# Optimization experiments

Hardware: AMD Instinct MI355X
Metric: run time of the kernel (lower is better)

## Reference

```python
import jax, jax.numpy as jnp
import numpy as np

D_MODEL = 256
N_HEADS = 8
HEAD_DIM = D_MODEL // N_HEADS


def setup_inputs() -> dict:
    key = jax.random.key(0)
    ks = jax.random.split(key, 10)
    B, L, D = 2, 2048, D_MODEL
    s = 1.0 / np.sqrt(D)
    inp = {
        "x": jax.random.normal(ks[0], (B, L, D), dtype=jnp.float32),
        "Wq": jax.random.normal(ks[1], (D, D), dtype=jnp.float32) * s,
        "bq": jnp.zeros((D,), jnp.float32),
        "Wk": jax.random.normal(ks[2], (D, D), dtype=jnp.float32) * s,
        "bk": jnp.zeros((D,), jnp.float32),
        "Wv": jax.random.normal(ks[3], (D, D), dtype=jnp.float32) * s,
        "bv": jnp.zeros((D,), jnp.float32),
        "u": jax.random.normal(ks[4], (N_HEADS, 1, 1), dtype=jnp.float32) * 0.1,
        "Wo": jax.random.normal(ks[5], (D, D), dtype=jnp.float32) * s,
        "bo": jnp.zeros((D,), jnp.float32),
    }
    return inp


def reference(x, Wq, bq, Wk, bk, Wv, bv, u, Wo, bo):
    B, L, D = x.shape
    H, hd = N_HEADS, HEAD_DIM

    def proj(W, b):  # torch Linear: x @ W.T + b -> [B,H,L,hd]
        return (x @ W.T + b).reshape(B, L, H, hd).transpose(0, 2, 1, 3)

    Q, K, V = proj(Wq, bq), proj(Wk, bk), proj(Wv, bv)

    scores = jnp.einsum("bhqd,bhkd->bhqk", Q, K) / np.sqrt(hd)
    attn_series = jax.nn.softmax(scores, axis=-1)  # [B,H,L,L]

    pos = jnp.arange(L, dtype=jnp.float32)
    dist = jnp.abs(pos[None, :] - pos[:, None])  # [L,L]
    # prior per head: exp(-d^2 / (2*(u^2+1e-6))), normalized over last dim
    prior = jnp.exp(-(dist[None] ** 2) / (2.0 * (u ** 2 + 1e-6)))  # [H,L,L]
    prior = prior / (prior.sum(axis=-1, keepdims=True) + 1e-6)

    discrepancy = jnp.abs(attn_series - prior[None]).mean(axis=(1, 2))  # [B,L]

    out = jnp.einsum("bhqk,bhkd->bhqd", attn_series, V)
    out = out.transpose(0, 2, 1, 3).reshape(B, L, D)
    out = out @ Wo.T + bo
    return out, discrepancy
```

## Files before the change

kernel.cpp:

```cpp
#include <hip/hip_runtime.h>
#include <hip/hip_bf16.h>
#include <math.h>

#define LSEQ 2048
#define DMODEL 256
#define NH 8
#define HD 32

typedef __attribute__((ext_vector_type(8))) short bf16x8;
typedef __attribute__((ext_vector_type(4))) float f32x4;

#define MFMA __builtin_amdgcn_mfma_f32_16x16x32_bf16

__device__ __forceinline__ short f2bf(float x) {
  __hip_bfloat16 h = __float2bfloat16(x);
  return __builtin_bit_cast(short, h);
}
__device__ __forceinline__ float bf2f(short s) {
  __hip_bfloat16 h = __builtin_bit_cast(__hip_bfloat16, s);
  return __bfloat162float(h);
}
__device__ __forceinline__ short bftrunc(float x) {
  return (short)(__builtin_bit_cast(unsigned int, x) >> 16);
}
__device__ __forceinline__ float fexp2(float x) {
#if __has_builtin(__builtin_amdgcn_exp2f)
  return __builtin_amdgcn_exp2f(x);
#else
  return __expf(x * 0.6931471805599453f);
#endif
}
__device__ __forceinline__ float flog2(float x) {
#if __has_builtin(__builtin_amdgcn_logf)
  return __builtin_amdgcn_logf(x);
#else
  return __logf(x) * 1.4426950408889634f;
#endif
}

__global__ __launch_bounds__(256) void aux_kernel(
    const float* __restrict__ Wq, const float* __restrict__ Wk,
    const float* __restrict__ Wv, const float* __restrict__ Wo,
    const float* __restrict__ u,
    short* __restrict__ Wch, short* __restrict__ Wcl,
    short* __restrict__ Woh, short* __restrict__ Wol,
    float* __restrict__ Eb, float* __restrict__ Zb,
    float* __restrict__ disc)
{
  __shared__ float Cs[LSEQ];
  __shared__ float part[256];
  const int tid = threadIdx.x;
  if (blockIdx.x < 256) {
    const int i4 = (blockIdx.x * 256 + tid) * 4;
    const float* src; short* dh; short* dl;
    if (i4 < 196608) {
      int row = i4 >> 8, col = i4 & 255;
      const float* W = (row < 256) ? Wq : (row < 512) ? Wk : Wv;
      src = W + (row & 255) * 256 + col; dh = Wch + i4; dl = Wcl + i4;
    } else {
      int j = i4 - 196608; src = Wo + j; dh = Woh + j; dl = Wol + j;
    }
    float4 v = *(const float4*)src;
    short h0 = f2bf(v.x), h1 = f2bf(v.y), h2 = f2bf(v.z), h3 = f2bf(v.w);
    *(short4*)dh = make_short4(h0, h1, h2, h3);
    *(short4*)dl = make_short4(bftrunc(v.x - bf2f(h0)), bftrunc(v.y - bf2f(h1)),
                               bftrunc(v.z - bf2f(h2)), bftrunc(v.w - bf2f(h3)));
    return;
  }
  const int h = blockIdx.x - 256;
  const float uu = u[h];
  const float den = 2.0f * (uu * uu + 1e-6f);
  float e[8]; float run = 0.f;
  const int base = tid * 8;
#pragma unroll
  for (int j = 0; j < 8; ++j) {
    float d = (float)(base + j);
    e[j] = __expf(-(d * d) / den);
    run += e[j];
  }
  part[tid] = run;
  __syncthreads();
  for (int off = 1; off < 256; off <<= 1) {
    float v = (tid >= off) ? part[tid - off] : 0.f;
    __syncthreads();
    part[tid] += v;
    __syncthreads();
  }
  float c = part[tid] - run;
#pragma unroll
  for (int j = 0; j < 8; ++j) {
    c += e[j];
    Cs[base + j] = c;
    Eb[h * LSEQ + base + j] = e[j];
  }
  __syncthreads();
  const float E0 = Cs[0];
  for (int i = tid; i < LSEQ; i += 256) {
    float s = Cs[i] + Cs[LSEQ - 1 - i] - E0;
    Zb[h * LSEQ + i] = 1.0f / (s + 1e-6f);
  }
  for (int i = tid; i < 512; i += 256) disc[h * 512 + i] = 0.f;
}

__global__ __launch_bounds__(256) void qkv_gemm(
    const float* __restrict__ x,
    const short* __restrict__ Bh, const short* __restrict__ Bl,
    const float* __restrict__ bq, const float* __restrict__ bk,
    const float* __restrict__ bv,
    short* __restrict__ Qf, short* __restrict__ Kf, short* __restrict__ Vf)
{
  const int tid = threadIdx.x, w = tid >> 6, lane = tid & 63;
  const int l15 = lane & 15, q4 = lane >> 4;
  const int m0 = blockIdx.x * 64, n0 = blockIdx.y * 64;
  const int mrow = m0 + w * 16 + l15;
  f32x4 acc[4] = {{0,0,0,0},{0,0,0,0},{0,0,0,0},{0,0,0,0}};
  for (int k0 = 0; k0 < 256; k0 += 32) {
    const float* xp = &x[(size_t)mrow * 256 + k0 + q4 * 8];
    float4 a = *(const float4*)xp;
    float4 c = *(const float4*)(xp + 4);
    float av[8] = {a.x,a.y,a.z,a.w,c.x,c.y,c.z,c.w};
    bf16x8 ah, al;
#pragma unroll
    for (int j = 0; j < 8; ++j) {
      short hi = f2bf(av[j]);
      ah[j] = hi;
      al[j] = bftrunc(av[j] - bf2f(hi));
    }
#pragma unroll
    for (int nt = 0; nt < 4; ++nt) {
      const size_t bi = (size_t)(n0 + nt * 16 + l15) * 256 + k0 + q4 * 8;
      bf16x8 bh = *(const bf16x8*)&Bh[bi];
      bf16x8 bl = *(const bf16x8*)&Bl[bi];
      acc[nt] = MFMA(ah, bh, acc[nt], 0, 0, 0);
      acc[nt] = MFMA(al, bh, acc[nt], 0, 0, 0);
      acc[nt] = MFMA(ah, bl, acc[nt], 0, 0, 0);
    }
  }
  const int type = n0 >> 8;
  const int n0l = n0 & 255;
  const float* bias = (type == 0) ? bq : (type == 1) ? bk : bv;
  const float qls = 0.25503489f;
#pragma unroll
  for (int nt = 0; nt < 4; ++nt) {
    const int col = n0l + nt * 16 + l15;
    const float bvv = bias[col];
    const int hh = col >> 5, dloc = col & 31;
#pragma unroll
    for (int r = 0; r < 4; ++r) {
      const int m = m0 + w * 16 + q4 * 4 + r;
      float v = acc[nt][r] + bvv;
      const int bb = m >> 11, mm = m & 2047, rr = mm & 15;
      if (type == 2) {
        const int kt128 = mm >> 7, low7 = mm & 127;
        const int wv = (low7 >> 4) & 3, ph = low7 >> 6;
        const int c = ph * 16 + rr;
        const size_t idx =
          ((((((size_t)bb * 8 + hh) * 16 + kt128) * 4 + wv) * 2 + (dloc >> 4)) * 64
           + (c >> 3) * 16 + (dloc & 15)) * 8 + (c & 7);
        Vf[idx] = f2bf(v);
      } else if (type == 0) {
        const int qblk = mm >> 5, rg = (mm >> 4) & 1;
        const size_t idx =
          (((((size_t)bb * 8 + hh) * 64 + qblk) * 2 + rg) * 64
           + (dloc >> 3) * 16 + rr) * 8 + (dloc & 7);
        Qf[idx] = f2bf(v * qls);
      } else {
        const int g = mm >> 4;
        const size_t idx =
          ((((size_t)bb * 8 + hh) * 128 + g) * 64
           + (dloc >> 3) * 16 + rr) * 8 + (dloc & 7);
        Kf[idx] = f2bf(v);
      }
    }
  }
}

__global__ __launch_bounds__(256) void out_gemm(
    const short* __restrict__ Ah, const short* __restrict__ Al,
    const short* __restrict__ Bh, const short* __restrict__ Bl,
    const float* __restrict__ bias, float* __restrict__ C)
{
  const int tid = threadIdx.x, w = tid >> 6, lane = tid & 63;
  const int l15 = lane & 15, q4 = lane >> 4;
  const int m0 = blockIdx.x * 64, n0 = blockIdx.y * 64;
  const int mrow = m0 + w * 16 + l15;
  f32x4 acc[4] = {{0,0,0,0},{0,0,0,0},{0,0,0,0},{0,0,0,0}};
  for (int k0 = 0; k0 < 256; k0 += 32) {
    bf16x8 ah = *(const bf16x8*)&Ah[(size_t)mrow * 256 + k0 + q4 * 8];
    bf16x8 al = *(const bf16x8*)&Al[(size_t)mrow * 256 + k0 + q4 * 8];
#pragma unroll
    for (int nt = 0; nt < 4; ++nt) {
      const size_t bi = (size_t)(n0 + nt * 16 + l15) * 256 + k0 + q4 * 8;
      bf16x8 bh = *(const bf16x8*)&Bh[bi];
      bf16x8 bl = *(const bf16x8*)&Bl[bi];
      acc[nt] = MFMA(ah, bh, acc[nt], 0, 0, 0);
      acc[nt] = MFMA(al, bh, acc[nt], 0, 0, 0);
      acc[nt] = MFMA(ah, bl, acc[nt], 0, 0, 0);
    }
  }
#pragma unroll
  for (int nt = 0; nt < 4; ++nt) {
    const int col = n0 + nt * 16 + l15;
    const float bvv = bias[col];
#pragma unroll
    for (int r = 0; r < 4; ++r) {
      const int m = m0 + w * 16 + q4 * 4 + r;
      C[(size_t)m * 256 + col] = acc[nt][r] + bvv;
    }
  }
}

__global__ __launch_bounds__(256) void attn_kernel(
    const short* __restrict__ Qf, const short* __restrict__ Kf,
    const short* __restrict__ Vf,
    const float* __restrict__ Eb, const float* __restrict__ Zb,
    short* __restrict__ Ohb, short* __restrict__ Olb,
    float* __restrict__ disc)
{
  __shared__ short Pt[4][32][40];
  __shared__ float Elds[192];
  __shared__ float dcol[LSEQ];
  __shared__ float lpart[4][32];

  const int tid = threadIdx.x, w = tid >> 6, lane = tid & 63;
  const int l15 = lane & 15, q4 = lane >> 4;
  const int flat = blockIdx.x + 64 * (blockIdx.y + 8 * blockIdx.z);
  const int slot = flat >> 3;
  const int g = (flat & 7) | ((slot >> 6) << 3);
  const int h = g & 7, b = g >> 3;
  const int q0 = (slot & 63) * 32;
  const int bh = b * NH + h;

  for (int i = tid; i < LSEQ; i += 256) dcol[i] = 0.f;
  if (tid < 192) Elds[tid] = Eb[h * LSEQ + tid];

  const bf16x8* Qf8 = (const bf16x8*)Qf;
  const bf16x8* Kf8 = (const bf16x8*)Kf;
  const bf16x8* Vf8 = (const bf16x8*)Vf;

  bf16x8 qh[2];
  float iz[2][4];
#pragma unroll
  for (int rg = 0; rg < 2; ++rg) {
    qh[rg] = Qf8[((((size_t)bh * 64 + (q0 >> 5)) * 2 + rg)) * 64 + lane];
#pragma unroll
    for (int r = 0; r < 4; ++r) iz[rg][r] = Zb[h * LSEQ + q0 + rg * 16 + q4 * 4 + r];
  }
  __syncthreads();

  const size_t kfb = (size_t)bh * 128;
  const size_t vfb = (size_t)bh * 16;

  float lac[2][4] = {{0,0,0,0},{0,0,0,0}};
#pragma unroll 2
  for (int kt = 0; kt < LSEQ; kt += 128) {
    bf16x8 k0 = Kf8[(kfb + (kt >> 4) + w) * 64 + lane];
    bf16x8 k1 = Kf8[(kfb + (kt >> 4) + 4 + w) * 64 + lane];
#pragma unroll
    for (int rg = 0; rg < 2; ++rg) {
      f32x4 s0 = {0.f, 0.f, 0.f, 0.f};
      s0 = MFMA(qh[rg], k0, s0, 0, 0, 0);
      f32x4 s1 = {0.f, 0.f, 0.f, 0.f};
      s1 = MFMA(qh[rg], k1, s1, 0, 0, 0);
#pragma unroll
      for (int r = 0; r < 4; ++r) lac[rg][r] += fexp2(s0[r]) + fexp2(s1[r]);
    }
  }
#pragma unroll
  for (int rg = 0; rg < 2; ++rg)
#pragma unroll
    for (int r = 0; r < 4; ++r) {
      float v = lac[rg][r];
      v += __shfl_xor(v, 1); v += __shfl_xor(v, 2);
      v += __shfl_xor(v, 4); v += __shfl_xor(v, 8);
      lac[rg][r] = v;
    }
  if (l15 == 0) {
#pragma unroll
    for (int rg = 0; rg < 2; ++rg)
#pragma unroll
      for (int r = 0; r < 4; ++r) lpart[w][rg * 16 + q4 * 4 + r] = lac[rg][r];
  }
  __syncthreads();
  f32x4 sinit[2];
#pragma unroll
  for (int rg = 0; rg < 2; ++rg)
#pragma unroll
    for (int r = 0; r < 4; ++r) {
      const int qi = rg * 16 + q4 * 4 + r;
      sinit[rg][r] = -flog2(lpart[0][qi] + lpart[1][qi] + lpart[2][qi] + lpart[3][qi]);
    }

  f32x4 oacc[2][2] = {{{0,0,0,0},{0,0,0,0}},{{0,0,0,0},{0,0,0,0}}};
#pragma unroll 2
  for (int kt = 0; kt < LSEQ; kt += 128) {
    bf16x8 kh0 = Kf8[(kfb + (kt >> 4) + w) * 64 + lane];
    bf16x8 kh1 = Kf8[(kfb + (kt >> 4) + 4 + w) * 64 + lane];
    bf16x8 vb[2];
#pragma unroll
    for (int dt = 0; dt < 2; ++dt)
      vb[dt] = Vf8[(((vfb + (kt >> 7)) * 4 + w) * 2 + dt) * 64 + lane];
#pragma unroll
    for (int ph = 0; ph < 2; ++ph) {
      bf16x8 kbh = ph ? kh1 : kh0;
      const int c0 = kt + ph * 64 + w * 16;
      const int kg = c0 + l15;
      const int dd = c0 - q0;
      const bool near = (dd >= -96) && (dd <= 96);
      float dsum = 0.f;
#pragma unroll
      for (int rg = 0; rg < 2; ++rg) {
        f32x4 s = sinit[rg];
        s = MFMA(qh[rg], kbh, s, 0, 0, 0);
#pragma unroll
        for (int r = 0; r < 4; ++r) {
          float p = fexp2(s[r]);
          Pt[w][rg * 16 + q4 * 4 + r][ph * 16 + l15] = bftrunc(p);
          if (near) {
            int qrow = q0 + rg * 16 + q4 * 4 + r;
            int dist = (qrow >= kg) ? (qrow - kg) : (kg - qrow);
            dsum += fabsf(p - Elds[dist] * iz[rg][r]);
          } else {
            dsum += p;
          }
        }
      }
      dsum += __shfl_xor(dsum, 16);
      dsum += __shfl_xor(dsum, 32);
      if (q4 == 0) atomicAdd(&dcol[kg], dsum);
    }
#pragma unroll
    for (int rg = 0; rg < 2; ++rg) {
      bf16x8 pa = *(const bf16x8*)&Pt[w][rg * 16 + l15][q4 * 8];
#pragma unroll
      for (int dt = 0; dt < 2; ++dt)
        oacc[rg][dt] = MFMA(pa, vb[dt], oacc[rg][dt], 0, 0, 0);
    }
  }

  __syncthreads();
  float* Ored = (float*)&Pt[0][0][0];
#pragma unroll
  for (int dt = 0; dt < 2; ++dt) {
#pragma unroll
    for (int rg = 0; rg < 2; ++rg)
#pragma unroll
      for (int r = 0; r < 4; ++r)
        Ored[(w * 32 + rg * 16 + q4 * 4 + r) * 17 + l15] = oacc[rg][dt][r];
    __syncthreads();
    for (int t = tid; t < 512; t += 256) {
      const int q = t >> 4, d = t & 15;
      float v = Ored[(q) * 17 + d] + Ored[(32 + q) * 17 + d] +
                Ored[(64 + q) * 17 + d] + Ored[(96 + q) * 17 + d];
      const size_t oo = ((size_t)b * LSEQ + q0 + q) * DMODEL + h * HD + dt * 16 + d;
      short hi = f2bf(v);
      Ohb[oo] = hi;
      Olb[oo] = bftrunc(v - bf2f(hi));
    }
    __syncthreads();
  }
  const float sc = 1.0f / (float)(NH * LSEQ);
  for (int i = tid; i < LSEQ; i += 256)
    atomicAdd(&disc[(size_t)b * LSEQ + i], dcol[i] * sc);
}

extern "C" void kernel_launch(void* const* d_in, const int* in_sizes, int n_in,
                              void* d_out, int out_size, void* d_ws, size_t ws_size,
                              hipStream_t stream)
{
  const float* x  = (const float*)d_in[0];
  const float* Wq = (const float*)d_in[1];
  const float* bq = (const float*)d_in[2];
  const float* Wk = (const float*)d_in[3];
  const float* bk = (const float*)d_in[4];
  const float* Wv = (const float*)d_in[5];
  const float* bv = (const float*)d_in[6];
  const float* u  = (const float*)d_in[7];
  const float* Wo = (const float*)d_in[8];
  const float* bo = (const float*)d_in[9];

  float* out  = (float*)d_out;
  float* disc = out + (size_t)2 * LSEQ * DMODEL;

  char* w8 = (char*)d_ws;
  const size_t MB = 1u << 20;
  short* Qfb = (short*)(w8);
  short* Kfb = (short*)(w8 + 2 * MB);
  short* Vfb = (short*)(w8 + 4 * MB);
  short* Ohb = (short*)(w8 + 6 * MB);
  short* Olb = (short*)(w8 + 8 * MB);
  short* Wch = (short*)(w8 + 10 * MB);
  short* Wcl = (short*)(w8 + 10 * MB + 393216);
  short* Woh = (short*)(w8 + 10 * MB + 786432);
  short* Wol = (short*)(w8 + 10 * MB + 917504);
  float* Eb  = (float*)(w8 + 11 * MB);
  float* Zb  = (float*)(w8 + 11 * MB + 65536);

  aux_kernel<<<264, 256, 0, stream>>>(Wq, Wk, Wv, Wo, u, Wch, Wcl, Woh, Wol,
                                      Eb, Zb, disc);
  qkv_gemm<<<dim3(64, 12), 256, 0, stream>>>(x, Wch, Wcl, bq, bk, bv,
                                             Qfb, Kfb, Vfb);
  attn_kernel<<<dim3(LSEQ / 32, NH, 2), 256, 0, stream>>>(Qfb, Kfb, Vfb,
                                                          Eb, Zb, Ohb, Olb, disc);
  out_gemm<<<dim3(64, 4), 256, 0, stream>>>(Ohb, Olb, Woh, Wol, bo, out);
}
```

Before: 171.1 us.

## Use single bf16 pass for QKV projection and tighten attention register use

```diff
diff --git a/kernel.cpp b/kernel.cpp
--- a/kernel.cpp
+++ b/kernel.cpp
@@ -42,7 +42,7 @@
     const float* __restrict__ Wq, const float* __restrict__ Wk,
     const float* __restrict__ Wv, const float* __restrict__ Wo,
     const float* __restrict__ u,
-    short* __restrict__ Wch, short* __restrict__ Wcl,
+    short* __restrict__ Wh,
     short* __restrict__ Woh, short* __restrict__ Wol,
     float* __restrict__ Eb, float* __restrict__ Zb,
     float* __restrict__ disc)
@@ -52,19 +52,19 @@
   const int tid = threadIdx.x;
   if (blockIdx.x < 256) {
     const int i4 = (blockIdx.x * 256 + tid) * 4;
-    const float* src; short* dh; short* dl;
     if (i4 < 196608) {
       int row = i4 >> 8, col = i4 & 255;
       const float* W = (row < 256) ? Wq : (row < 512) ? Wk : Wv;
-      src = W + (row & 255) * 256 + col; dh = Wch + i4; dl = Wcl + i4;
+      float4 v = *(const float4*)(W + (row & 255) * 256 + col);
+      *(short4*)(Wh + i4) = make_short4(f2bf(v.x), f2bf(v.y), f2bf(v.z), f2bf(v.w));
     } else {
-      int j = i4 - 196608; src = Wo + j; dh = Woh + j; dl = Wol + j;
-    }
-    float4 v = *(const float4*)src;
-    short h0 = f2bf(v.x), h1 = f2bf(v.y), h2 = f2bf(v.z), h3 = f2bf(v.w);
-    *(short4*)dh = make_short4(h0, h1, h2, h3);
-    *(short4*)dl = make_short4(bftrunc(v.x - bf2f(h0)), bftrunc(v.y - bf2f(h1)),
-                               bftrunc(v.z - bf2f(h2)), bftrunc(v.w - bf2f(h3)));
+      int j = i4 - 196608;
+      float4 v = *(const float4*)(Wo + j);
+      short h0 = f2bf(v.x), h1 = f2bf(v.y), h2 = f2bf(v.z), h3 = f2bf(v.w);
+      *(short4*)(Woh + j) = make_short4(h0, h1, h2, h3);
+      *(short4*)(Wol + j) = make_short4(bftrunc(v.x - bf2f(h0)), bftrunc(v.y - bf2f(h1)),
+                                        bftrunc(v.z - bf2f(h2)), bftrunc(v.w - bf2f(h3)));
+    }
     return;
   }
   const int h = blockIdx.x - 256;
@@ -104,7 +104,7 @@
 
 __global__ __launch_bounds__(256) void qkv_gemm(
     const float* __restrict__ x,
-    const short* __restrict__ Bh, const short* __restrict__ Bl,
+    const short* __restrict__ Bh,
     const float* __restrict__ bq, const float* __restrict__ bk,
     const float* __restrict__ bv,
     short* __restrict__ Qf, short* __restrict__ Kf, short* __restrict__ Vf)
@@ -118,22 +118,14 @@
     const float* xp = &x[(size_t)mrow * 256 + k0 + q4 * 8];
     float4 a = *(const float4*)xp;
     float4 c = *(const float4*)(xp + 4);
-    float av[8] = {a.x,a.y,a.z,a.w,c.x,c.y,c.z,c.w};
-    bf16x8 ah, al;
-#pragma unroll
-    for (int j = 0; j < 8; ++j) {
-      short hi = f2bf(av[j]);
-      ah[j] = hi;
-      al[j] = bftrunc(av[j] - bf2f(hi));
-    }
+    bf16x8 ah;
+    ah[0] = f2bf(a.x); ah[1] = f2bf(a.y); ah[2] = f2bf(a.z); ah[3] = f2bf(a.w);
+    ah[4] = f2bf(c.x); ah[5] = f2bf(c.y); ah[6] = f2bf(c.z); ah[7] = f2bf(c.w);
 #pragma unroll
     for (int nt = 0; nt < 4; ++nt) {
       const size_t bi = (size_t)(n0 + nt * 16 + l15) * 256 + k0 + q4 * 8;
       bf16x8 bh = *(const bf16x8*)&Bh[bi];
-      bf16x8 bl = *(const bf16x8*)&Bl[bi];
       acc[nt] = MFMA(ah, bh, acc[nt], 0, 0, 0);
-      acc[nt] = MFMA(al, bh, acc[nt], 0, 0, 0);
-      acc[nt] = MFMA(ah, bl, acc[nt], 0, 0, 0);
     }
   }
   const int type = n0 >> 8;
@@ -210,7 +202,7 @@
   }
 }
 
-__global__ __launch_bounds__(256) void attn_kernel(
+__global__ __launch_bounds__(256, 4) void attn_kernel(
     const short* __restrict__ Qf, const short* __restrict__ Kf,
     const short* __restrict__ Vf,
     const float* __restrict__ Eb, const float* __restrict__ Zb,
@@ -221,6 +213,7 @@
   __shared__ float Elds[192];
   __shared__ float dcol[LSEQ];
   __shared__ float lpart[4][32];
+  __shared__ float izlds[32];
 
   const int tid = threadIdx.x, w = tid >> 6, lane = tid & 63;
   const int l15 = lane & 15, q4 = lane >> 4;
@@ -233,19 +226,16 @@
 
   for (int i = tid; i < LSEQ; i += 256) dcol[i] = 0.f;
   if (tid < 192) Elds[tid] = Eb[h * LSEQ + tid];
+  if (tid < 32)  izlds[tid] = Zb[h * LSEQ + q0 + tid];
 
   const bf16x8* Qf8 = (const bf16x8*)Qf;
   const bf16x8* Kf8 = (const bf16x8*)Kf;
   const bf16x8* Vf8 = (const bf16x8*)Vf;
 
   bf16x8 qh[2];
-  float iz[2][4];
-#pragma unroll
-  for (int rg = 0; rg < 2; ++rg) {
+#pragma unroll
+  for (int rg = 0; rg < 2; ++rg)
     qh[rg] = Qf8[((((size_t)bh * 64 + (q0 >> 5)) * 2 + rg)) * 64 + lane];
-#pragma unroll
-    for (int r = 0; r < 4; ++r) iz[rg][r] = Zb[h * LSEQ + q0 + rg * 16 + q4 * 4 + r];
-  }
   __syncthreads();
 
   const size_t kfb = (size_t)bh * 128;
@@ -296,10 +286,8 @@
   for (int kt = 0; kt < LSEQ; kt += 128) {
     bf16x8 kh0 = Kf8[(kfb + (kt >> 4) + w) * 64 + lane];
     bf16x8 kh1 = Kf8[(kfb + (kt >> 4) + 4 + w) * 64 + lane];
-    bf16x8 vb[2];
-#pragma unroll
-    for (int dt = 0; dt < 2; ++dt)
-      vb[dt] = Vf8[(((vfb + (kt >> 7)) * 4 + w) * 2 + dt) * 64 + lane];
+    bf16x8 vb0 = Vf8[(((vfb + (kt >> 7)) * 4 + w) * 2 + 0) * 64 + lane];
+    bf16x8 vb1 = Vf8[(((vfb + (kt >> 7)) * 4 + w) * 2 + 1) * 64 + lane];
 #pragma unroll
     for (int ph = 0; ph < 2; ++ph) {
       bf16x8 kbh = ph ? kh1 : kh0;
@@ -319,7 +307,7 @@
           if (near) {
             int qrow = q0 + rg * 16 + q4 * 4 + r;
             int dist = (qrow >= kg) ? (qrow - kg) : (kg - qrow);
-            dsum += fabsf(p - Elds[dist] * iz[rg][r]);
+            dsum += fabsf(p - Elds[dist] * izlds[rg * 16 + q4 * 4 + r]);
           } else {
             dsum += p;
           }
@@ -332,9 +320,8 @@
 #pragma unroll
     for (int rg = 0; rg < 2; ++rg) {
       bf16x8 pa = *(const bf16x8*)&Pt[w][rg * 16 + l15][q4 * 8];
-#pragma unroll
-      for (int dt = 0; dt < 2; ++dt)
-        oacc[rg][dt] = MFMA(pa, vb[dt], oacc[rg][dt], 0, 0, 0);
+      oacc[rg][0] = MFMA(pa, vb0, oacc[rg][0], 0, 0, 0);
+      oacc[rg][1] = MFMA(pa, vb1, oacc[rg][1], 0, 0, 0);
     }
   }
 
@@ -389,16 +376,15 @@
   short* Vfb = (short*)(w8 + 4 * MB);
   short* Ohb = (short*)(w8 + 6 * MB);
   short* Olb = (short*)(w8 + 8 * MB);
-  short* Wch = (short*)(w8 + 10 * MB);
-  short* Wcl = (short*)(w8 + 10 * MB + 393216);
-  short* Woh = (short*)(w8 + 10 * MB + 786432);
-  short* Wol = (short*)(w8 + 10 * MB + 917504);
+  short* Wh  = (short*)(w8 + 10 * MB);
+  short* Woh = (short*)(w8 + 10 * MB + 393216);
+  short* Wol = (short*)(w8 + 10 * MB + 524288);
   float* Eb  = (float*)(w8 + 11 * MB);
   float* Zb  = (float*)(w8 + 11 * MB + 65536);
 
-  aux_kernel<<<264, 256, 0, stream>>>(Wq, Wk, Wv, Wo, u, Wch, Wcl, Woh, Wol,
+  aux_kernel<<<264, 256, 0, stream>>>(Wq, Wk, Wv, Wo, u, Wh, Woh, Wol,
                                       Eb, Zb, disc);
-  qkv_gemm<<<dim3(64, 12), 256, 0, stream>>>(x, Wch, Wcl, bq, bk, bv,
+  qkv_gemm<<<dim3(64, 12), 256, 0, stream>>>(x, Wh, bq, bk, bv,
                                              Qfb, Kfb, Vfb);
   attn_kernel<<<dim3(LSEQ / 32, NH, 2), 256, 0, stream>>>(Qfb, Kfb, Vfb,
                                                           Eb, Zb, Ohb, Olb, disc);
```

Result: faster. 158.6 us (median of 2 runs) (-7.3%).
